# Kernel tuning notes

Hardware: AMD Instinct MI355X
Metric: run time of the kernel (lower is better)

Reference implementation:

```python
import jax, jax.numpy as jnp
import numpy as np

B, T, D, N = 256, 512, 512, 64


def setup_inputs() -> dict:
    key = jax.random.key(0)
    ks = jax.random.split(key, 8)
    s = 0.05  # keep gate pre-activations in a sane range
    return {
        "x": jax.random.normal(ks[0], (B, T, D), dtype=jnp.float32),
        "init_h": jax.random.normal(ks[1], (B, D), dtype=jnp.float32) * s,
        "W_ih": jax.random.normal(ks[2], (4 * D, D + N), dtype=jnp.float32) * s,
        "b_ih": jax.random.normal(ks[3], (4 * D,), dtype=jnp.float32) * s,
        "W_hh": jax.random.normal(ks[4], (4 * D, D), dtype=jnp.float32) * s,
        "b_hh": jax.random.normal(ks[5], (4 * D,), dtype=jnp.float32) * s,
        "W_lin": jax.random.normal(ks[6], (N, D), dtype=jnp.float32) * s,
        "b_lin": jax.random.normal(ks[7], (N,), dtype=jnp.float32) * s,
    }


def reference(x, init_h, W_ih, b_ih, W_hh, b_hh, W_lin, b_lin):
    n_class = W_lin.shape[0]
    d = init_h.shape[-1]

    def step(carry, x_t):
        h, c, y = carry
        inp = jnp.concatenate([x_t, y], axis=-1)  # [B, D+N]
        gates = inp @ W_ih.T + b_ih + h @ W_hh.T + b_hh  # [B, 4D]
        i, f, g, o = jnp.split(gates, 4, axis=-1)
        i = jax.nn.sigmoid(i)
        f = jax.nn.sigmoid(f)
        g = jnp.tanh(g)
        o = jax.nn.sigmoid(o)
        c = f * c + i * g
        h = o * jnp.tanh(c)
        y = jax.nn.softmax(h @ W_lin.T + b_lin, axis=-1)  # [B, N]
        return (h, c, y), y

    c0 = jnp.zeros_like(init_h)
    y0 = jnp.zeros((x.shape[0], n_class), dtype=x.dtype)
    xs = jnp.swapaxes(x, 0, 1)  # [T, B, D]
    _, ys = jax.lax.scan(step, (init_h, c0, y0), xs)  # ys: [T, B, N]
    return jnp.swapaxes(ys, 0, 1)  # [B, T, N]
```

## Files before the change

### kernel.cpp

```cpp
#include <hip/hip_runtime.h>
#include <cstdint>
#include <cstddef>


typedef _Float16 f16x8 __attribute__((ext_vector_type(8)));
typedef float f32x4 __attribute__((ext_vector_type(4)));

#define MFMA16(a, b, c_) __builtin_amdgcn_mfma_f32_16x16x32_f16((a), (b), (c_), 0, 0, 0)
#define AGT __HIP_MEMORY_SCOPE_AGENT
#define RLX __ATOMIC_RELAXED

#define FLAG_INTS (256 * 64 + 64)
#define HS2_U32 131072

static __device__ __forceinline__ unsigned short f2b(_Float16 h) {
  return __builtin_bit_cast(unsigned short, h);
}
static __device__ __forceinline__ _Float16 b2f(unsigned short s) {
  return __builtin_bit_cast(_Float16, s);
}

__device__ __forceinline__ void cvt8(const float4 a, const float4 b, f16x8& hi, f16x8& lo) {
  float v[8] = {a.x, a.y, a.z, a.w, b.x, b.y, b.z, b.w};
#pragma unroll
  for (int j = 0; j < 8; ++j) {
    _Float16 h = (_Float16)v[j];
    hi[j] = h;
    lo[j] = (_Float16)(v[j] - (float)h);
  }
}

template <bool XPRE>
__global__ void prep_kernel(const float* __restrict__ x, const float* __restrict__ init_h,
                            const float* __restrict__ W_ih, const float* __restrict__ b_ih,
                            const float* __restrict__ W_hh, const float* __restrict__ b_hh,
                            _Float16* __restrict__ xs, _Float16* __restrict__ wf,
                            unsigned int* __restrict__ hs2, float* __restrict__ bias,
                            int* __restrict__ flags) {
  const long NX = XPRE ? 256L * 512 * 16 * 4 : 0;
  const int NWF = 128 * 34 * 64;
  const int NH2 = 256 * 16 * 4;
  long tid = (long)blockIdx.x * 256 + threadIdx.x;

  if (XPRE && tid < NX) {
    int q = tid & 3, ki = (tid >> 2) & 15, t = (tid >> 6) & 511;
    int row = (int)(tid >> 15);
    const float* s = x + (((size_t)row * 512 + t) * 512 + ki * 32 + 4 * q);
    float4 a = *(const float4*)s, b = *(const float4*)(s + 16);
    f16x8 hi, lo;
    cvt8(a, b, hi, lo);
    _Float16* d = xs + ((((size_t)row * 512 + t) * 16 + ki) * 64 + q * 16);
    *(f16x8*)d = hi;
    *(f16x8*)(d + 8) = lo;
    return;
  }
  long u = tid - NX;
  if (u >= 0 && u < NWF) {
    int l = (int)(u & 63);
    int u2 = (int)(u >> 6);
    int ki = u2 % 34, ct = u2 / 34;
    int cb = ct >> 1, cth = ct & 1;
    int l15 = l & 15;
    int col = (l15 >> 2) * 512 + cb * 8 + cth * 4 + (l15 & 3);
    int k = ki * 32 + 4 * (l >> 4);
    float4 a, b;
    if (k < 512) {
      const float* p = W_ih + (size_t)col * 576;
      a = *(const float4*)(p + k);
      b = *(const float4*)(p + k + 16);
    } else if (k < 1024) {
      const float* p = W_hh + (size_t)col * 512;
      a = *(const float4*)(p + k - 512);
      b = *(const float4*)(p + k - 512 + 16);
    } else {
      const float* p = W_ih + (size_t)col * 576 + 512;
      a = *(const float4*)(p + k - 1024);
      b = *(const float4*)(p + k - 1024 + 16);
    }
    f16x8 hi, lo;
    cvt8(a, b, hi, lo);
    _Float16* d = wf + (((size_t)ct * 34 + ki) * 64 + l) * 16;
    *(f16x8*)d = hi;
    *(f16x8*)(d + 8) = lo;
    return;
  }
  u -= NWF;
  if (u >= 0 && u < NH2) {
    int q = (int)(u & 3), ki = (int)((u >> 2) & 15), row = (int)(u >> 6);
    const float* s = init_h + ((size_t)row * 512 + ki * 32 + 4 * q);
    float4 a = *(const float4*)s, b = *(const float4*)(s + 16);
    float v[8] = {a.x, a.y, a.z, a.w, b.x, b.y, b.z, b.w};
    unsigned int pk[8];
#pragma unroll
    for (int j = 0; j < 8; ++j) {
      _Float16 hh = (_Float16)v[j];
      _Float16 hl = (_Float16)(v[j] - (float)hh);
      pk[j] = (unsigned int)f2b(hh) | ((unsigned int)f2b(hl) << 16);
    }
    unsigned int* base = hs2 + ((size_t)row * 16 + ki) * 32;
    *(uint4*)(base + 4 * q) = make_uint4(pk[0], pk[1], pk[2], pk[3]);
    *(uint4*)(base + 16 + 4 * q) = make_uint4(pk[4], pk[5], pk[6], pk[7]);
    return;
  }
  u -= NH2;
  if (u >= 0 && u < 2048) {
    bias[u] = b_ih[u] + b_hh[u];
    return;
  }
  u -= 2048;
  if (u >= 0 && u < FLAG_INTS) flags[u] = 0;
}

#define GKSTEP(AH, AL, KI)                                                   \
  {                                                                          \
    const _Float16* B0p = wfl + (size_t)(KI)*1024 + (size_t)l * 16;          \
    const _Float16* B1p = B0p + 34 * 1024;                                   \
    f16x8 b0h = *(const f16x8*)B0p, b0l = *(const f16x8*)(B0p + 8);          \
    f16x8 b1h = *(const f16x8*)B1p, b1l = *(const f16x8*)(B1p + 8);          \
    aC0 = MFMA16((AH), b0h, aC0);                                            \
    aC1 = MFMA16((AH), b1h, aC1);                                            \
    aC0 = MFMA16((AL), b0h, aC0);                                            \
    aC1 = MFMA16((AL), b1h, aC1);                                            \
    aC0 = MFMA16((AH), b0l, aC0);                                            \
    aC1 = MFMA16((AH), b1l, aC1);                                            \
  }

template <bool XPRE>
__global__ void __launch_bounds__(512, 2) recur_kernel(
    const float* __restrict__ x, const float* __restrict__ b_lin,
    const float* __restrict__ W_lin, const _Float16* __restrict__ xs,
    const _Float16* __restrict__ wf, unsigned int* __restrict__ hs2,
    const float* __restrict__ bias, float* __restrict__ out, float* __restrict__ ylog,
    int* __restrict__ flags) {
  const int bid = blockIdx.x;
  const int x8 = bid & 7;
  const int g = x8 >> 1;
  const int cb = (x8 & 1) * 32 + (bid >> 3);
  const int tid = threadIdx.x;
  const int l = tid & 63, w = tid >> 6;
  const int l15 = l & 15, q = l >> 4;
  const int kh = w & 1, rtp = w >> 1;

  __shared__ _Float16 wfl[2 * 34 * 64 * 16];
  __shared__ float pacc[4][2][4][64];
  __shared__ float lp[4][16];
  __shared__ int s_ab;

  {
    const _Float16* srcw = wf + (size_t)cb * (2 * 34 * 64 * 16);
#pragma unroll
    for (int i = 0; i < 17; ++i) {
      int idx = tid + i * 512;
      *(float4*)(wfl + (size_t)idx * 8) = *(const float4*)(srcw + (size_t)idx * 8);
    }
    if (tid == 0) s_ab = 0;
  }
  __syncthreads();

  const int dd = l15 & 3, rr = l15 >> 2;
  float bg[2][4];
#pragma unroll
  for (int c2 = 0; c2 < 2; ++c2)
#pragma unroll
    for (int gi = 0; gi < 4; ++gi) bg[c2][gi] = bias[gi * 512 + cb * 8 + c2 * 4 + dd];
  const float blin = b_lin[cb];

  const int Rw = g * 64 + rtp * 16;
  const int rowA = Rw + l15;
  const int hoff = rowA * 512 + 4 * q;
  const _Float16* xsA = xs + (size_t)rowA * 524288 + q * 16;
  const float* xfA = x + (size_t)rowA * 262144 + 4 * q;
  const float* wl = W_lin + (size_t)cb * 512;

  const int rowE = Rw + 4 * q + rr;
  unsigned int hwo[2];
#pragma unroll
  for (int c2 = 0; c2 < 2; ++c2) {
    int dglob = cb * 8 + c2 * 4 + dd;
    int kiH = dglob >> 5, k32 = dglob & 31;
    int e = 4 * ((k32 & 15) >> 2) + (k32 & 3) + 16 * (k32 >> 4);
    hwo[c2] = (unsigned int)((rowE * 16 + kiH) * 32 + e);
  }

  int* abortf = flags + 256 * 64;

  auto BAR = [&](int target) -> bool {
    __syncthreads();
    if (tid == 0)
      __hip_atomic_store(flags + (size_t)(g * 64 + cb) * 64, target, RLX, AGT);
    if (tid < 64) {
      int a = 0;
      int* f = flags + ((size_t)g * 64 + tid) * 64;
      int it = 0;
      while (__hip_atomic_load(f, RLX, AGT) < target) {
        __builtin_amdgcn_s_sleep(1);
        if (++it > 400000) {
          a = 1;
          break;
        }
        if ((it & 255) == 0 && __hip_atomic_load(abortf, RLX, AGT) != 0) {
          a = 1;
          break;
        }
      }
      a = __any(a) ? 1 : 0;
      if (tid == 0) {
        if (a) __hip_atomic_store(abortf, 1, RLX, AGT);
        s_ab = a;
      }
    }
    __syncthreads();
    return s_ab != 0;
  };

  float cst[2] = {0.f, 0.f};
  f32x4 aC0, aC1;

#pragma unroll 1
  for (int s = 0; s < 512; ++s) {
    aC0 = (f32x4){0.f, 0.f, 0.f, 0.f};
    aC1 = (f32x4){0.f, 0.f, 0.f, 0.f};

    if (XPRE) {
      const _Float16* xA = xsA + (size_t)s * 1024;
#pragma unroll
      for (int i = 0; i < 8; ++i) {
        int kx = kh * 8 + i;
        f16x8 ah = *(const f16x8*)(xA + kx * 64);
        f16x8 al = *(const f16x8*)(xA + kx * 64 + 8);
        GKSTEP(ah, al, kx);
      }
    } else {
      const float* xp = xfA + (size_t)s * 512;
#pragma unroll 2
      for (int i = 0; i < 8; ++i) {
        int kx = kh * 8 + i;
        float4 av = *(const float4*)(xp + kx * 32);
        float4 bv = *(const float4*)(xp + kx * 32 + 16);
        f16x8 ah, al;
        cvt8(av, bv, ah, al);
        GKSTEP(ah, al, kx);
      }
    }

    if (s > 0) {
      if (BAR(2 * s)) return;
    }

    const unsigned int* hp0 = hs2 + (size_t)(s & 1) * HS2_U32 + hoff;
    float dlg = 0.f;
#pragma unroll
    for (int i = 0; i < 8; ++i) {
      int kk = kh * 8 + i;
      const unsigned int* hp = hp0 + kk * 32;
      unsigned long long u0 = __hip_atomic_load((const unsigned long long*)hp, RLX, AGT);
      unsigned long long u1 = __hip_atomic_load((const unsigned long long*)(hp + 2), RLX, AGT);
      unsigned long long u2 = __hip_atomic_load((const unsigned long long*)(hp + 16), RLX, AGT);
      unsigned long long u3 = __hip_atomic_load((const unsigned long long*)(hp + 18), RLX, AGT);
      unsigned int wd[8] = {(unsigned int)u0, (unsigned int)(u0 >> 32),
                            (unsigned int)u1, (unsigned int)(u1 >> 32),
                            (unsigned int)u2, (unsigned int)(u2 >> 32),
                            (unsigned int)u3, (unsigned int)(u3 >> 32)};
      f16x8 ah, al;
#pragma unroll
      for (int j = 0; j < 8; ++j) {
        ah[j] = b2f((unsigned short)(wd[j] & 0xffffu));
        al[j] = b2f((unsigned short)(wd[j] >> 16));
      }
      GKSTEP(ah, al, 16 + kk);
      float4 wa = *(const float4*)(wl + kk * 32 + 4 * q);
      float4 wb2 = *(const float4*)(wl + kk * 32 + 16 + 4 * q);
      dlg += ((float)ah[0] + (float)al[0]) * wa.x + ((float)ah[1] + (float)al[1]) * wa.y +
             ((float)ah[2] + (float)al[2]) * wa.z + ((float)ah[3] + (float)al[3]) * wa.w +
             ((float)ah[4] + (float)al[4]) * wb2.x + ((float)ah[5] + (float)al[5]) * wb2.y +
             ((float)ah[6] + (float)al[6]) * wb2.z + ((float)ah[7] + (float)al[7]) * wb2.w;
    }
    dlg += __shfl_xor(dlg, 16);
    dlg += __shfl_xor(dlg, 32);
    if (kh == 1 && l < 16) lp[rtp][l15] = dlg;
    __syncthreads();
    if (kh == 0 && l < 16) {
      float full = dlg + lp[rtp][l15] + blin;
      __hip_atomic_store(ylog + ((size_t)g * 64 + cb) * 64 + rtp * 16 + l15, full, RLX, AGT);
    }

    if (BAR(2 * s + 1)) return;

    if (s > 0) {
      float la[4][4];
#pragma unroll
      for (int b2 = 0; b2 < 4; ++b2)
#pragma unroll
        for (int m = 0; m < 4; ++m)
          la[b2][m] = __hip_atomic_load(
              ylog + ((size_t)g * 64 + 16 * b2 + 4 * q + m) * 64 + rtp * 16 + l15, RLX, AGT);
      float mx = la[0][0];
#pragma unroll
      for (int b2 = 0; b2 < 4; ++b2)
#pragma unroll
        for (int m = 0; m < 4; ++m) mx = fmaxf(mx, la[b2][m]);
      mx = fmaxf(mx, __shfl_xor(mx, 16));
      mx = fmaxf(mx, __shfl_xor(mx, 32));
      float sm = 0.f;
#pragma unroll
      for (int b2 = 0; b2 < 4; ++b2)
#pragma unroll
        for (int m = 0; m < 4; ++m) {
          la[b2][m] = __expf(la[b2][m] - mx);
          sm += la[b2][m];
        }
      sm += __shfl_xor(sm, 16);
      sm += __shfl_xor(sm, 32);
      float inv = 1.f / sm;
      if (cb == 0 && kh == 0) {
        size_t ob = (((size_t)(g * 64 + rtp * 16 + l15)) * 512 + (s - 1)) * 64;
#pragma unroll
        for (int b2 = 0; b2 < 4; ++b2)
#pragma unroll
          for (int m = 0; m < 4; ++m) out[ob + 16 * b2 + 4 * q + m] = la[b2][m] * inv;
      }
      f16x8 yh;
      if (kh == 0) {
#pragma unroll
        for (int j = 0; j < 8; ++j) yh[j] = (_Float16)(la[j >> 2][j & 3] * inv);
      } else {
#pragma unroll
        for (int j = 0; j < 8; ++j) yh[j] = (_Float16)(la[(j >> 2) + 2][j & 3] * inv);
      }
      const _Float16* B0p = wfl + (size_t)(32 + kh) * 1024 + (size_t)l * 16;
      const _Float16* B1p = B0p + 34 * 1024;
      f16x8 b0h = *(const f16x8*)B0p, b0l = *(const f16x8*)(B0p + 8);
      f16x8 b1h = *(const f16x8*)B1p, b1l = *(const f16x8*)(B1p + 8);
      aC0 = MFMA16(yh, b0h, aC0);
      aC1 = MFMA16(yh, b1h, aC1);
      aC0 = MFMA16(yh, b0l, aC0);
      aC1 = MFMA16(yh, b1l, aC1);
    }

    if (kh == 1) {
#pragma unroll
      for (int r = 0; r < 4; ++r) {
        pacc[rtp][0][r][l] = aC0[r];
        pacc[rtp][1][r][l] = aC1[r];
      }
    }
    __syncthreads();
    if (kh == 0) {
#pragma unroll
      for (int r = 0; r < 4; ++r) {
        aC0[r] += pacc[rtp][0][r][l];
        aC1[r] += pacc[rtp][1][r][l];
      }
      const unsigned int wb_ = (unsigned int)(((s & 1) ^ 1) * HS2_U32);
#pragma unroll
      for (int c2 = 0; c2 < 2; ++c2) {
        f32x4 A = c2 ? aC1 : aC0;
        float z[4];
#pragma unroll
        for (int gi = 0; gi < 4; ++gi) {
          int src = (l & 48) | (gi * 4 + dd);
          float v0 = __shfl(A[0], src), v1 = __shfl(A[1], src);
          float v2 = __shfl(A[2], src), v3 = __shfl(A[3], src);
          z[gi] = (rr == 0) ? v0 : (rr == 1) ? v1 : (rr == 2) ? v2 : v3;
        }
        float zi = z[0] + bg[c2][0], zf = z[1] + bg[c2][1];
        float zg = z[2] + bg[c2][2], zo = z[3] + bg[c2][3];
        float iv = 1.f / (1.f + __expf(-zi));
        float fv = 1.f / (1.f + __expf(-zf));
        float eg = __expf(2.f * zg);
        float gv = 1.f - 2.f / (eg + 1.f);
        float ov = 1.f / (1.f + __expf(-zo));
        float cn = fv * cst[c2] + iv * gv;
        cst[c2] = cn;
        float ec = __expf(2.f * cn);
        float th = 1.f - 2.f / (ec + 1.f);
        float hv = ov * th;
        _Float16 hh = (_Float16)hv;
        _Float16 hl = (_Float16)(hv - (float)hh);
        unsigned int pk = (unsigned int)f2b(hh) | ((unsigned int)f2b(hl) << 16);
        __hip_atomic_store(hs2 + wb_ + hwo[c2], pk, RLX, AGT);
      }
    }
  }

  if (BAR(1024)) return;
  {
    const unsigned int* hp0 = hs2 + hoff;
    float dlg = 0.f;
#pragma unroll
    for (int i = 0; i < 8; ++i) {
      int kk = kh * 8 + i;
      const unsigned int* hp = hp0 + kk * 32;
      unsigned long long u0 = __hip_atomic_load((const unsigned long long*)hp, RLX, AGT);
      unsigned long long u1 = __hip_atomic_load((const unsigned long long*)(hp + 2), RLX, AGT);
      unsigned long long u2 = __hip_atomic_load((const unsigned long long*)(hp + 16), RLX, AGT);
      unsigned long long u3 = __hip_atomic_load((const unsigned long long*)(hp + 18), RLX, AGT);
      unsigned int wd[8] = {(unsigned int)u0, (unsigned int)(u0 >> 32),
                            (unsigned int)u1, (unsigned int)(u1 >> 32),
                            (unsigned int)u2, (unsigned int)(u2 >> 32),
                            (unsigned int)u3, (unsigned int)(u3 >> 32)};
      float4 wa = *(const float4*)(wl + kk * 32 + 4 * q);
      float4 wb2 = *(const float4*)(wl + kk * 32 + 16 + 4 * q);
      float hv0[8];
#pragma unroll
      for (int j = 0; j < 8; ++j)
        hv0[j] = (float)b2f((unsigned short)(wd[j] & 0xffffu)) +
                 (float)b2f((unsigned short)(wd[j] >> 16));
      dlg += hv0[0] * wa.x + hv0[1] * wa.y + hv0[2] * wa.z + hv0[3] * wa.w + hv0[4] * wb2.x +
             hv0[5] * wb2.y + hv0[6] * wb2.z + hv0[7] * wb2.w;
    }
    dlg += __shfl_xor(dlg, 16);
    dlg += __shfl_xor(dlg, 32);
    if (kh == 1 && l < 16) lp[rtp][l15] = dlg;
    __syncthreads();
    if (kh == 0 && l < 16)
      __hip_atomic_store(ylog + ((size_t)g * 64 + cb) * 64 + rtp * 16 + l15,
                         dlg + lp[rtp][l15] + blin, RLX, AGT);
  }
  if (BAR(1025)) return;
  if (cb == 0 && kh == 0) {
    float la[4][4];
#pragma unroll
    for (int b2 = 0; b2 < 4; ++b2)
#pragma unroll
      for (int m = 0; m < 4; ++m)
        la[b2][m] = __hip_atomic_load(
            ylog + ((size_t)g * 64 + 16 * b2 + 4 * q + m) * 64 + rtp * 16 + l15, RLX, AGT);
    float mx = la[0][0];
#pragma unroll
    for (int b2 = 0; b2 < 4; ++b2)
#pragma unroll
      for (int m = 0; m < 4; ++m) mx = fmaxf(mx, la[b2][m]);
    mx = fmaxf(mx, __shfl_xor(mx, 16));
    mx = fmaxf(mx, __shfl_xor(mx, 32));
    float sm = 0.f;
#pragma unroll
    for (int b2 = 0; b2 < 4; ++b2)
#pragma unroll
      for (int m = 0; m < 4; ++m) {
        la[b2][m] = __expf(la[b2][m] - mx);
        sm += la[b2][m];
      }
    sm += __shfl_xor(sm, 16);
    sm += __shfl_xor(sm, 32);
    float inv = 1.f / sm;
    size_t ob = (((size_t)(g * 64 + rtp * 16 + l15)) * 512 + 511) * 64;
#pragma unroll
    for (int b2 = 0; b2 < 4; ++b2)
#pragma unroll
      for (int m = 0; m < 4; ++m) out[ob + 16 * b2 + 4 * q + m] = la[b2][m] * inv;
  }
}

extern "C" void kernel_launch(void* const* d_in, const int* in_sizes, int n_in, void* d_out,
                              int out_size, void* d_ws, size_t ws_size, hipStream_t stream) {
  const float* x = (const float*)d_in[0];
  const float* init_h = (const float*)d_in[1];
  const float* W_ih = (const float*)d_in[2];
  const float* b_ih = (const float*)d_in[3];
  const float* W_hh = (const float*)d_in[4];
  const float* b_hh = (const float*)d_in[5];
  const float* W_lin = (const float*)d_in[6];
  const float* b_lin = (const float*)d_in[7];
  float* out = (float*)d_out;
  (void)in_sizes;
  (void)n_in;
  (void)out_size;

  char* ws = (char*)d_ws;
  size_t off = 0;
  auto take = [&](size_t bytes) -> char* {
    char* r = ws + off;
    off = (off + bytes + 255) & ~(size_t)255;
    return r;
  };
  const size_t WF_E = (size_t)128 * 34 * 64 * 16;
  const size_t XS_E = (size_t)256 * 512 * 16 * 64;

  _Float16* wf = (_Float16*)take(WF_E * 2);
  unsigned int* hs2 = (unsigned int*)take((size_t)2 * HS2_U32 * 4);
  float* bias = (float*)take(2048 * 4);
  float* ylogb = (float*)take((size_t)4 * 64 * 64 * 4);
  int* flags = (int*)take((size_t)FLAG_INTS * 4);
  if (ws_size < off) return;
  _Float16* xs = (_Float16*)(ws + off);
  const bool xpre = (ws_size >= off + XS_E * 2);

  if (xpre) {
    const long total = 8388608L + 278528 + 16384 + 2048 + FLAG_INTS;
    prep_kernel<true><<<(int)((total + 255) / 256), 256, 0, stream>>>(
        x, init_h, W_ih, b_ih, W_hh, b_hh, xs, wf, hs2, bias, flags);
    recur_kernel<true><<<256, 512, 0, stream>>>(x, b_lin, W_lin, xs, wf, hs2, bias, out, ylogb,
                                                flags);
  } else {
    const long total = 278528L + 16384 + 2048 + FLAG_INTS;
    prep_kernel<false><<<(int)((total + 255) / 256), 256, 0, stream>>>(
        x, init_h, W_ih, b_ih, W_hh, b_hh, xs, wf, hs2, bias, flags);
    recur_kernel<false><<<256, 512, 0, stream>>>(x, b_lin, W_lin, xs, wf, hs2, bias, out, ylogb,
                                                 flags);
  }
}
```

Before: 9.496 ms.

## Split grid barrier into arrive/wait and overlap h-MFMAs with logit barrier

Splits the cross-block barrier into separate arrive and wait phases. After publishing the logits, each block now arrives first and then runs the recurrent h-by-W_hh MFMAs before waiting, so that matmul work hides the barrier latency. It also splits the shared-memory weight tile into separate hi and lo arrays, and loads all h values into registers up front. The cost is higher register pressure from holding 16 f16x8 h fragments, plus some added complexity in the barrier protocol ordering.

```diff
diff --git a/kernel.cpp b/kernel.cpp
--- a/kernel.cpp
+++ b/kernel.cpp
@@ -111,18 +111,18 @@
   if (u >= 0 && u < FLAG_INTS) flags[u] = 0;
 }
 
-#define GKSTEP(AH, AL, KI)                                                   \
-  {                                                                          \
-    const _Float16* B0p = wfl + (size_t)(KI)*1024 + (size_t)l * 16;          \
-    const _Float16* B1p = B0p + 34 * 1024;                                   \
-    f16x8 b0h = *(const f16x8*)B0p, b0l = *(const f16x8*)(B0p + 8);          \
-    f16x8 b1h = *(const f16x8*)B1p, b1l = *(const f16x8*)(B1p + 8);          \
-    aC0 = MFMA16((AH), b0h, aC0);                                            \
-    aC1 = MFMA16((AH), b1h, aC1);                                            \
-    aC0 = MFMA16((AL), b0h, aC0);                                            \
-    aC1 = MFMA16((AL), b1h, aC1);                                            \
-    aC0 = MFMA16((AH), b0l, aC0);                                            \
-    aC1 = MFMA16((AH), b1l, aC1);                                            \
+#define GKSTEP(AH, AL, KI)                                                       \
+  {                                                                              \
+    const f16x8 b0h = *(const f16x8*)(wfl_hi + ((size_t)(KI)*64 + l) * 8);       \
+    const f16x8 b1h = *(const f16x8*)(wfl_hi + 17408 + ((size_t)(KI)*64 + l) * 8); \
+    const f16x8 b0l = *(const f16x8*)(wfl_lo + ((size_t)(KI)*64 + l) * 8);       \
+    const f16x8 b1l = *(const f16x8*)(wfl_lo + 17408 + ((size_t)(KI)*64 + l) * 8); \
+    aC0 = MFMA16((AH), b0h, aC0);                                                \
+    aC1 = MFMA16((AH), b1h, aC1);                                                \
+    aC0 = MFMA16((AL), b0h, aC0);                                                \
+    aC1 = MFMA16((AL), b1h, aC1);                                                \
+    aC0 = MFMA16((AH), b0l, aC0);                                                \
+    aC1 = MFMA16((AH), b1l, aC1);                                                \
   }
 
 template <bool XPRE>
@@ -141,17 +141,22 @@
   const int l15 = l & 15, q = l >> 4;
   const int kh = w & 1, rtp = w >> 1;
 
-  __shared__ _Float16 wfl[2 * 34 * 64 * 16];
+  __shared__ _Float16 wfl_hi[2 * 34 * 64 * 8];
+  __shared__ _Float16 wfl_lo[2 * 34 * 64 * 8];
   __shared__ float pacc[4][2][4][64];
   __shared__ float lp[4][16];
   __shared__ int s_ab;
 
   {
-    const _Float16* srcw = wf + (size_t)cb * (2 * 34 * 64 * 16);
-#pragma unroll
-    for (int i = 0; i < 17; ++i) {
-      int idx = tid + i * 512;
-      *(float4*)(wfl + (size_t)idx * 8) = *(const float4*)(srcw + (size_t)idx * 8);
+    const _Float16* srcw = wf + (size_t)cb * 4352 * 16;
+#pragma unroll
+    for (int i = 0; i < 9; ++i) {
+      int u = tid + i * 512;
+      if (u < 4352) {
+        const float4* s16 = (const float4*)(srcw + (size_t)u * 16);
+        *(float4*)(wfl_hi + (size_t)u * 8) = s16[0];
+        *(float4*)(wfl_lo + (size_t)u * 8) = s16[1];
+      }
     }
     if (tid == 0) s_ab = 0;
   }
@@ -184,15 +189,16 @@
 
   int* abortf = flags + 256 * 64;
 
-  auto BAR = [&](int target) -> bool {
+  auto ARRIVE = [&](int v) {
     __syncthreads();
-    if (tid == 0)
-      __hip_atomic_store(flags + (size_t)(g * 64 + cb) * 64, target, RLX, AGT);
+    if (tid == 0) __hip_atomic_store(flags + (size_t)(g * 64 + cb) * 64, v, RLX, AGT);
+  };
+  auto WAIT = [&](int v) -> bool {
     if (tid < 64) {
       int a = 0;
       int* f = flags + ((size_t)g * 64 + tid) * 64;
       int it = 0;
-      while (__hip_atomic_load(f, RLX, AGT) < target) {
+      while (__hip_atomic_load(f, RLX, AGT) < v) {
         __builtin_amdgcn_s_sleep(1);
         if (++it > 400000) {
           a = 1;
@@ -244,15 +250,14 @@
     }
 
     if (s > 0) {
-      if (BAR(2 * s)) return;
+      if (WAIT(2 * s)) return;
     }
 
     const unsigned int* hp0 = hs2 + (size_t)(s & 1) * HS2_U32 + hoff;
-    float dlg = 0.f;
+    f16x8 hh[8], hl[8];
 #pragma unroll
     for (int i = 0; i < 8; ++i) {
-      int kk = kh * 8 + i;
-      const unsigned int* hp = hp0 + kk * 32;
+      const unsigned int* hp = hp0 + (kh * 8 + i) * 32;
       unsigned long long u0 = __hip_atomic_load((const unsigned long long*)hp, RLX, AGT);
       unsigned long long u1 = __hip_atomic_load((const unsigned long long*)(hp + 2), RLX, AGT);
       unsigned long long u2 = __hip_atomic_load((const unsigned long long*)(hp + 16), RLX, AGT);
@@ -261,19 +266,27 @@
                             (unsigned int)u1, (unsigned int)(u1 >> 32),
                             (unsigned int)u2, (unsigned int)(u2 >> 32),
                             (unsigned int)u3, (unsigned int)(u3 >> 32)};
-      f16x8 ah, al;
 #pragma unroll
       for (int j = 0; j < 8; ++j) {
-        ah[j] = b2f((unsigned short)(wd[j] & 0xffffu));
-        al[j] = b2f((unsigned short)(wd[j] >> 16));
-      }
-      GKSTEP(ah, al, 16 + kk);
+        hh[i][j] = b2f((unsigned short)(wd[j] & 0xffffu));
+        hl[i][j] = b2f((unsigned short)(wd[j] >> 16));
+      }
+    }
+
+    float dlg = 0.f;
+#pragma unroll
+    for (int i = 0; i < 8; ++i) {
+      int kk = kh * 8 + i;
       float4 wa = *(const float4*)(wl + kk * 32 + 4 * q);
       float4 wb2 = *(const float4*)(wl + kk * 32 + 16 + 4 * q);
-      dlg += ((float)ah[0] + (float)al[0]) * wa.x + ((float)ah[1] + (float)al[1]) * wa.y +
-             ((float)ah[2] + (float)al[2]) * wa.z + ((float)ah[3] + (float)al[3]) * wa.w +
-             ((float)ah[4] + (float)al[4]) * wb2.x + ((float)ah[5] + (float)al[5]) * wb2.y +
-             ((float)ah[6] + (float)al[6]) * wb2.z + ((float)ah[7] + (float)al[7]) * wb2.w;
+      dlg += ((float)hh[i][0] + (float)hl[i][0]) * wa.x +
+             ((float)hh[i][1] + (float)hl[i][1]) * wa.y +
+             ((float)hh[i][2] + (float)hl[i][2]) * wa.z +
+             ((float)hh[i][3] + (float)hl[i][3]) * wa.w +
+             ((float)hh[i][4] + (float)hl[i][4]) * wb2.x +
+             ((float)hh[i][5] + (float)hl[i][5]) * wb2.y +
+             ((float)hh[i][6] + (float)hl[i][6]) * wb2.z +
+             ((float)hh[i][7] + (float)hl[i][7]) * wb2.w;
     }
     dlg += __shfl_xor(dlg, 16);
     dlg += __shfl_xor(dlg, 32);
@@ -283,8 +296,12 @@
       float full = dlg + lp[rtp][l15] + blin;
       __hip_atomic_store(ylog + ((size_t)g * 64 + cb) * 64 + rtp * 16 + l15, full, RLX, AGT);
     }
-
-    if (BAR(2 * s + 1)) return;
+    ARRIVE(2 * s + 1);
+
+#pragma unroll
+    for (int i = 0; i < 8; ++i) GKSTEP(hh[i], hl[i], 16 + kh * 8 + i);
+
+    if (WAIT(2 * s + 1)) return;
 
     if (s > 0) {
       float la[4][4];
@@ -327,10 +344,11 @@
 #pragma unroll
         for (int j = 0; j < 8; ++j) yh[j] = (_Float16)(la[(j >> 2) + 2][j & 3] * inv);
       }
-      const _Float16* B0p = wfl + (size_t)(32 + kh) * 1024 + (size_t)l * 16;
-      const _Float16* B1p = B0p + 34 * 1024;
-      f16x8 b0h = *(const f16x8*)B0p, b0l = *(const f16x8*)(B0p + 8);
-      f16x8 b1h = *(const f16x8*)B1p, b1l = *(const f16x8*)(B1p + 8);
+      const int KY = 32 + kh;
+      const f16x8 b0h = *(const f16x8*)(wfl_hi + ((size_t)KY * 64 + l) * 8);
+      const f16x8 b1h = *(const f16x8*)(wfl_hi + 17408 + ((size_t)KY * 64 + l) * 8);
+      const f16x8 b0l = *(const f16x8*)(wfl_lo + ((size_t)KY * 64 + l) * 8);
+      const f16x8 b1l = *(const f16x8*)(wfl_lo + 17408 + ((size_t)KY * 64 + l) * 8);
       aC0 = MFMA16(yh, b0h, aC0);
       aC1 = MFMA16(yh, b1h, aC1);
       aC0 = MFMA16(yh, b0l, aC0);
@@ -375,15 +393,16 @@
         float ec = __expf(2.f * cn);
         float th = 1.f - 2.f / (ec + 1.f);
         float hv = ov * th;
-        _Float16 hh = (_Float16)hv;
-        _Float16 hl = (_Float16)(hv - (float)hh);
-        unsigned int pk = (unsigned int)f2b(hh) | ((unsigned int)f2b(hl) << 16);
+        _Float16 hh2 = (_Float16)hv;
+        _Float16 hl2 = (_Float16)(hv - (float)hh2);
+        unsigned int pk = (unsigned int)f2b(hh2) | ((unsigned int)f2b(hl2) << 16);
         __hip_atomic_store(hs2 + wb_ + hwo[c2], pk, RLX, AGT);
       }
     }
-  }
-
-  if (BAR(1024)) return;
+    ARRIVE(2 * s + 2);
+  }
+
+  if (WAIT(1024)) return;
   {
     const unsigned int* hp0 = hs2 + hoff;
     float dlg = 0.f;
@@ -417,7 +436,8 @@
       __hip_atomic_store(ylog + ((size_t)g * 64 + cb) * 64 + rtp * 16 + l15,
                          dlg + lp[rtp][l15] + blin, RLX, AGT);
   }
-  if (BAR(1025)) return;
+  ARRIVE(1025);
+  if (WAIT(1025)) return;
   if (cb == 0 && kh == 0) {
     float la[4][4];
 #pragma unroll
```

New measurement: 8.857 ms. 1.07x faster.
